# Performance work log

Measured on AMD Instinct MI355X. Metric: run time of the kernel, lower is better.

Reference implementation:

```python
import jax, jax.numpy as jnp
import numpy as np


def setup_inputs() -> dict:
    key = jax.random.key(0)
    ks = jax.random.split(key, 7)
    B, T, I, H, O = 64, 2048, 32, 256, 32
    s = 0.05
    return {
        "x": jax.random.normal(ks[0], (B, T, I), dtype=jnp.float32),
        "W_ih": jax.random.normal(ks[1], (4 * H, I), dtype=jnp.float32) * s,
        "W_hh": jax.random.normal(ks[2], (4 * H, H), dtype=jnp.float32) * s,
        "b_ih": jax.random.normal(ks[3], (4 * H,), dtype=jnp.float32) * s,
        "b_hh": jax.random.normal(ks[4], (4 * H,), dtype=jnp.float32) * s,
        "fc_w": jax.random.normal(ks[5], (O, H), dtype=jnp.float32) * s,
        "fc_b": jax.random.normal(ks[6], (O,), dtype=jnp.float32) * s,
    }


def _lstm(x, W_ih, W_hh, b_ih, b_hh):
    # x: [B,T,I]; PyTorch gate order: i, f, g, o stacked along 4H axis.
    B = x.shape[0]
    H = W_hh.shape[1]
    # Precompute input contributions for all timesteps in one GEMM: [B,T,4H]
    xg = jnp.einsum('bti,gi->btg', x, W_ih) + b_ih + b_hh

    def step(carry, xg_t):
        h, c = carry  # [B,H] each
        gates = xg_t + h @ W_hh.T  # [B,4H]
        i, f, g, o = jnp.split(gates, 4, axis=-1)
        i = jax.nn.sigmoid(i)
        f = jax.nn.sigmoid(f)
        g = jnp.tanh(g)
        o = jax.nn.sigmoid(o)
        c = f * c + i * g
        h = o * jnp.tanh(c)
        return (h, c), h

    h0 = jnp.zeros((B, H), dtype=x.dtype)
    (_, _), hs = jax.lax.scan(step, (h0, h0), jnp.swapaxes(xg, 0, 1))
    return jnp.swapaxes(hs, 0, 1)  # [B,T,H]


def reference(x, W_ih, W_hh, b_ih, b_hh, fc_w, fc_b):
    out = _lstm(x, W_ih, W_hh, b_ih, b_hh)          # [B,T,H]
    # Conv1d(H, O, kernel_size=1) over channel dim == pointwise linear.
    return jnp.einsum('bth,oh->bto', out, fc_w) + fc_b  # [B,T,O]
```

## Files before the change

### kernel.cpp

```cpp
#include <hip/hip_runtime.h>
#include <cstdint>


#define B_  64
#define T_  2048
#define I_  32
#define H_  256
#define G4  1024
#define O_  32

typedef int v16i __attribute__((ext_vector_type(16)));
typedef int v4i  __attribute__((ext_vector_type(4)));
typedef _Float16 h2_t __attribute__((ext_vector_type(2)));

#if __has_builtin(__builtin_amdgcn_sdot4)
__device__ __forceinline__ int dot4(int a, int b, int c) {
    return __builtin_amdgcn_sdot4(a, b, c, false);
}
#else
__device__ __forceinline__ int dot4(int a, int b, int c) {
    c += (int)(int8_t)(a)        * (int)(int8_t)(b);
    c += (int)(int8_t)(a >> 8)   * (int)(int8_t)(b >> 8);
    c += (int)(int8_t)(a >> 16)  * (int)(int8_t)(b >> 16);
    c += (int)(int8_t)(a >> 24)  * (int)(int8_t)(b >> 24);
    return c;
}
#endif

__device__ __forceinline__ float fdot2h(h2_t a, h2_t b, float c) {
#if __has_builtin(__builtin_amdgcn_fdot2)
    return __builtin_amdgcn_fdot2(a, b, c, false);
#else
    return c + (float)a[0] * (float)b[0] + (float)a[1] * (float)b[1];
#endif
}

#define QWHH_OFF 0
#define QWIH_OFF 262144
#define S1_OFF   327680
#define S2_OFF   331776
#define BIAS_OFF 335872
#define XQ_OFF   339968
#define XS_OFF   8728576
#define HBUF_OFF 9252864
#define HREC_STRIDE 320
#define HSLOTS 2049

__device__ __forceinline__ uint32_t pack_q(int q0, int q1, int q2, int q3) {
    return  ((uint32_t)(uint8_t)(int8_t)q0)
          | (((uint32_t)(uint8_t)(int8_t)q1) << 8)
          | (((uint32_t)(uint8_t)(int8_t)q2) << 16)
          | (((uint32_t)(uint8_t)(int8_t)q3) << 24);
}

__device__ __forceinline__ int clamp127(int v) {
    return v < -127 ? -127 : (v > 127 ? 127 : v);
}

__global__ __launch_bounds__(64) void prep_w(
    const float* __restrict__ Whh, const float* __restrict__ Wih,
    const float* __restrict__ bih, const float* __restrict__ bhh,
    uint32_t* __restrict__ qwhh, uint32_t* __restrict__ qwih,
    float* __restrict__ s1, float* __restrict__ s2, float* __restrict__ bias)
{
    const int r = blockIdx.x;
    const int l = threadIdx.x;

    const float4 wv = ((const float4*)(Whh + r * H_))[l];
    float m = fmaxf(fmaxf(fabsf(wv.x), fabsf(wv.y)), fmaxf(fabsf(wv.z), fabsf(wv.w)));
    #pragma unroll
    for (int s = 1; s < 64; s <<= 1) m = fmaxf(m, __shfl_xor(m, s, 64));
    const float S1 = fmaxf(m, 1e-20f) / 127.f;

    float xm = (l < I_) ? fabsf(Wih[r * I_ + l]) : 0.f;
    #pragma unroll
    for (int s = 1; s < 64; s <<= 1) xm = fmaxf(xm, __shfl_xor(xm, s, 64));
    const float S2 = fmaxf(xm, 1e-20f) / 127.f;

    {
        const float r1 = 1.f / S1;
        qwhh[l * G4 + r] = pack_q(
            clamp127((int)rintf(wv.x * r1)), clamp127((int)rintf(wv.y * r1)),
            clamp127((int)rintf(wv.z * r1)), clamp127((int)rintf(wv.w * r1)));
    }
    if (l < 8) {
        const float4 xw = ((const float4*)(Wih + r * I_))[l];
        const float r2 = 1.f / S2;
        qwih[l * G4 + r] = pack_q(
            clamp127((int)rintf(xw.x * r2)), clamp127((int)rintf(xw.y * r2)),
            clamp127((int)rintf(xw.z * r2)), clamp127((int)rintf(xw.w * r2)));
    } else if (l < 16) {
        const int j = l - 8;
        const float4 xw = ((const float4*)(Wih + r * I_))[j];
        const float r2 = 1.f / S2;
        float v0 = xw.x * r2, v1 = xw.y * r2, v2 = xw.z * r2, v3 = xw.w * r2;
        int a0 = clamp127((int)rintf(v0)), a1 = clamp127((int)rintf(v1));
        int a2 = clamp127((int)rintf(v2)), a3 = clamp127((int)rintf(v3));
        qwih[(8 + j) * G4 + r] = pack_q(
            clamp127((int)rintf((v0 - (float)a0) * 127.f)),
            clamp127((int)rintf((v1 - (float)a1) * 127.f)),
            clamp127((int)rintf((v2 - (float)a2) * 127.f)),
            clamp127((int)rintf((v3 - (float)a3) * 127.f)));
    }
    if (l == 0) { s1[r] = S1; s2[r] = S2; bias[r] = bih[r] + bhh[r]; }
}

__global__ __launch_bounds__(256) void prep_x(
    const float* __restrict__ x, uint32_t* __restrict__ xq, float* __restrict__ xs)
{
    __shared__ float xb[64 * 32];
    const int base = blockIdx.x * 64 * 32;
    for (int i = threadIdx.x; i < 2048; i += 256) xb[i] = x[base + i];
    __syncthreads();
    const int t = threadIdx.x;
    if (t < 64) {
        float m = 0.f;
        for (int k = 0; k < 32; k++) m = fmaxf(m, fabsf(xb[t * 32 + k]));
        const float S = fmaxf(m, 1e-20f) / 127.f;
        const int row = blockIdx.x * 64 + t;
        xs[row] = S;
        const float rS = 1.f / S;
        for (int j = 0; j < 8; j++) {
            int qa[4], qb[4];
            for (int e = 0; e < 4; e++) {
                float v = xb[t * 32 + j * 4 + e] * rS;
                int a = clamp127((int)rintf(v));
                int b = clamp127((int)rintf((v - (float)a) * 127.f));
                qa[e] = a; qb[e] = b;
            }
            xq[row * 16 + j]     = pack_q(qa[0], qa[1], qa[2], qa[3]);
            xq[row * 16 + 8 + j] = pack_q(qb[0], qb[1], qb[2], qb[3]);
        }
    }
}

__device__ __forceinline__ float x_contrib(const uint32_t* pxq, const float* pxs,
                                           const uint32_t* wA, const uint32_t* wB,
                                           float S2, float bias_r) {
    v16i xv; int sxi;
    asm volatile("s_load_dwordx16 %0, %2, 0x0\n\t"
                 "s_load_dword %1, %3, 0x0\n\t"
                 "s_waitcnt lgkmcnt(0)"
                 : "=&s"(xv), "=&s"(sxi)
                 : "s"(pxq), "s"(pxs)
                 : "memory");
    int aA = 0, aM = 0;
    #pragma unroll
    for (int j = 0; j < 8; j++) {
        aA = dot4((int)wA[j], xv[j],     aA);
        aM = dot4((int)wA[j], xv[8 + j], aM);
        aM = dot4((int)wB[j], xv[j],     aM);
    }
    return ((float)aA + (float)aM * (1.f / 127.f)) * (S2 * __int_as_float(sxi)) + bias_r;
}

__global__ __launch_bounds__(1024, 4) void lstm_main(
    const uint32_t* __restrict__ qwhh, const uint32_t* __restrict__ qwih,
    const float* __restrict__ s1v, const float* __restrict__ s2v,
    const float* __restrict__ biasv,
    const uint32_t* __restrict__ xq, const float* __restrict__ xs,
    const float* __restrict__ fcw, const float* __restrict__ fcb,
    char* __restrict__ hbuf, float* __restrict__ out)
{
    const int b   = blockIdx.x;
    const int tid = threadIdx.x;

    __shared__ float    gbuf[768];
    __shared__ uint32_t hf16[128];

    uint32_t w[64], wA[8], wB[8];
    #pragma unroll
    for (int d = 0; d < 64; d++) w[d] = qwhh[d * G4 + tid];
    #pragma unroll
    for (int j = 0; j < 8; j++) { wA[j] = qwih[j * G4 + tid]; wB[j] = qwih[(8 + j) * G4 + tid]; }
    const float S1 = s1v[tid], S2 = s2v[tid], bias_r = biasv[tid];

    const int o_ = tid >> 5, kc = tid & 31;
    h2_t fw[4];
    {
        const float* fr = fcw + o_ * H_ + kc * 8;
        #pragma unroll
        for (int j = 0; j < 4; j++) {
            h2_t p; p[0] = (_Float16)fr[2 * j]; p[1] = (_Float16)fr[2 * j + 1];
            fw[j] = p;
        }
    }
    const float fcb_v = fcb[o_];

    char* hb = hbuf + (size_t)b * (HSLOTS * HREC_STRIDE);
    if (tid < H_) hb[2048 * HREC_STRIDE + tid] = 0;
    if (tid >= 256 && tid < 260) ((float*)(hb + 2048 * HREC_STRIDE + 256))[tid - 256] = 0.f;

    const uint32_t* xqb  = xq + (size_t)(b * T_) * 16;
    const float*    xsb  = xs + (size_t)(b * T_);
    float*          outb = out + (size_t)(b * T_) * O_;

    float c_state = 0.f;
    float x_part  = x_contrib(xqb, xsb, wA, wB, S2, bias_r);

    __syncthreads();

    for (int t = 0; t < T_; t++) {
        const uint32_t slot = (t == 0) ? 2048u : ((uint32_t)(t * 1993) & 2047u);
        const char* hrec = hb + (size_t)slot * HREC_STRIDE;
        v16i h0, h1, h2, h3; v4i scv;
        asm volatile("s_load_dwordx16 %0, %5, 0x0\n\t"
                     "s_load_dwordx16 %1, %5, 0x40\n\t"
                     "s_load_dwordx16 %2, %5, 0x80\n\t"
                     "s_load_dwordx16 %3, %5, 0xc0\n\t"
                     "s_load_dwordx4  %4, %5, 0x100\n\t"
                     "s_waitcnt lgkmcnt(0)"
                     : "=&s"(h0), "=&s"(h1), "=&s"(h2), "=&s"(h3), "=&s"(scv)
                     : "s"(hrec)
                     : "memory");

        int a0 = 0, a1 = 0, a2 = 0, a3 = 0;
        #pragma unroll
        for (int d = 0; d < 16; d++) {
            a0 = dot4((int)w[d],      h0[d], a0);
            a1 = dot4((int)w[16 + d], h1[d], a1);
            a2 = dot4((int)w[32 + d], h2[d], a2);
            a3 = dot4((int)w[48 + d], h3[d], a3);
        }
        const float hsum = (float)a0 * __int_as_float(scv[0])
                         + (float)a1 * __int_as_float(scv[1])
                         + (float)a2 * __int_as_float(scv[2])
                         + (float)a3 * __int_as_float(scv[3]);
        const float gate = hsum * S1 + x_part;

        if (tid >= 256) gbuf[tid - 256] = gate;
        __syncthreads();

        const uint32_t wslot = (uint32_t)((t + 1) * 1993) & 2047u;
        char* hw = hb + (size_t)wslot * HREC_STRIDE;
        float hval = 0.f;
        if (tid < H_) {
            const float gi = gate;
            const float gf = gbuf[tid];
            const float gg = gbuf[256 + tid];
            const float go = gbuf[512 + tid];
            const float i_ = 1.f / (1.f + __expf(-gi));
            const float f_ = 1.f / (1.f + __expf(-gf));
            const float g_ = 2.f / (1.f + __expf(-2.f * gg)) - 1.f;
            const float oo = 1.f / (1.f + __expf(-go));
            c_state = f_ * c_state + i_ * g_;
            const float tc = 2.f / (1.f + __expf(-2.f * c_state)) - 1.f;
            hval = oo * tc;
            ((_Float16*)hf16)[tid] = (_Float16)hval;

            float m = fabsf(hval);
            #pragma unroll
            for (int s = 1; s < 64; s <<= 1) m = fmaxf(m, __shfl_xor(m, s, 64));
            m = fmaxf(m, 1e-12f);
            const float rq = 127.f / m;
            const int q = clamp127((int)rintf(hval * rq));
            hw[tid] = (char)(int8_t)q;
            if ((tid & 63) == 0)
                ((float*)(hw + 256))[tid >> 6] = m * (1.f / 127.f);
        }

        if (t < T_ - 1)
            x_part = x_contrib(xqb + (size_t)(t + 1) * 16, xsb + (t + 1),
                               wA, wB, S2, bias_r);

        __syncthreads();

        {
            const uint4 hv = *(const uint4*)(&hf16[4 * kc]);
            union { uint32_t u; h2_t h; } u0, u1, u2, u3;
            u0.u = hv.x; u1.u = hv.y; u2.u = hv.z; u3.u = hv.w;
            float acc = 0.f;
            acc = fdot2h(fw[0], u0.h, acc);
            acc = fdot2h(fw[1], u1.h, acc);
            acc = fdot2h(fw[2], u2.h, acc);
            acc = fdot2h(fw[3], u3.h, acc);
            #pragma unroll
            for (int s = 1; s < 32; s <<= 1) acc += __shfl_xor(acc, s, 64);
            if (kc == 0) outb[t * O_ + o_] = acc + fcb_v;
        }
    }
}

extern "C" void kernel_launch(void* const* d_in, const int* in_sizes, int n_in,
                              void* d_out, int out_size, void* d_ws, size_t ws_size,
                              hipStream_t stream) {
    const float* x    = (const float*)d_in[0];
    const float* Wih  = (const float*)d_in[1];
    const float* Whh  = (const float*)d_in[2];
    const float* bih  = (const float*)d_in[3];
    const float* bhh  = (const float*)d_in[4];
    const float* fcw  = (const float*)d_in[5];
    const float* fcb  = (const float*)d_in[6];
    float* out = (float*)d_out;

    char* ws = (char*)d_ws;
    uint32_t* qwhh = (uint32_t*)(ws + QWHH_OFF);
    uint32_t* qwih = (uint32_t*)(ws + QWIH_OFF);
    float*    s1   = (float*)(ws + S1_OFF);
    float*    s2   = (float*)(ws + S2_OFF);
    float*    bias = (float*)(ws + BIAS_OFF);
    uint32_t* xq   = (uint32_t*)(ws + XQ_OFF);
    float*    xs   = (float*)(ws + XS_OFF);
    char*     hbuf = ws + HBUF_OFF;

    prep_w<<<G4, 64, 0, stream>>>(Whh, Wih, bih, bhh, qwhh, qwih, s1, s2, bias);
    prep_x<<<(B_ * T_) / 64, 256, 0, stream>>>(x, xq, xs);
    lstm_main<<<B_, 1024, 0, stream>>>(qwhh, qwih, s1, s2, bias, xq, xs,
                                       fcw, fcb, hbuf, out);
}
```

Measured before the change: 3.533 ms.

## Halve LSTM block size, precompute input gates, split FC into separate kernel

The recurrent kernel now uses 512 threads per batch, each computing two gate rows (i/g or f/o paired across half-waves via shuffles). This removes the shared-memory gate exchange and one barrier per step, at the cost of doubling per-thread weight registers. When the workspace is large enough, the input projection is precomputed in fp16 by a separate GEMM kernel and streamed in per step. The output linear layer moves out of the recurrent loop into a batched fc_kernel over stored fp16 hidden states, which adds extra memory traffic and launches.

```diff
diff --git a/kernel.cpp b/kernel.cpp
--- a/kernel.cpp
+++ b/kernel.cpp
@@ -10,7 +10,7 @@
 #define O_  32
 
 typedef int v16i __attribute__((ext_vector_type(16)));
-typedef int v4i  __attribute__((ext_vector_type(4)));
+typedef int v8i  __attribute__((ext_vector_type(8)));
 typedef _Float16 h2_t __attribute__((ext_vector_type(2)));
 
 #if __has_builtin(__builtin_amdgcn_sdot4)
@@ -35,16 +35,20 @@
 #endif
 }
 
-#define QWHH_OFF 0
-#define QWIH_OFF 262144
-#define S1_OFF   327680
-#define S2_OFF   331776
-#define BIAS_OFF 335872
-#define XQ_OFF   339968
-#define XS_OFF   8728576
-#define HBUF_OFF 9252864
+#define QWHH_OFF 0u
+#define QWIH_OFF 262144u
+#define S1_OFF   327680u
+#define S2_OFF   331776u
+#define BIAS_OFF 335872u
+#define HBUF_OFF 339968u
 #define HREC_STRIDE 320
 #define HSLOTS 2049
+#define HSTORE_OFF (339968u + 41963520u)
+#define XQ_OFF  (HSTORE_OFF + 67108864u)
+#define XS_OFF  (XQ_OFF + 8388608u)
+#define XG_OFF  (HSTORE_OFF + 67108864u)
+#define FULL_NEED  ((size_t)XG_OFF + 268435456ull)
+#define FB_NEED    ((size_t)XS_OFF + 524288ull)
 
 __device__ __forceinline__ uint32_t pack_q(int q0, int q1, int q2, int q3) {
     return  ((uint32_t)(uint8_t)(int8_t)q0)
@@ -52,10 +56,10 @@
           | (((uint32_t)(uint8_t)(int8_t)q2) << 16)
           | (((uint32_t)(uint8_t)(int8_t)q3) << 24);
 }
-
 __device__ __forceinline__ int clamp127(int v) {
     return v < -127 ? -127 : (v > 127 ? 127 : v);
 }
+
 
 __global__ __launch_bounds__(64) void prep_w(
     const float* __restrict__ Whh, const float* __restrict__ Wih,
@@ -65,6 +69,10 @@
 {
     const int r = blockIdx.x;
     const int l = threadIdx.x;
+    const int j = r & 255, g = r >> 8;
+    const int col = 64 * (j >> 5) + ((g & 1) ? 32 : 0) + (j & 31);
+    const int dbase = (g >= 2) ? 64 : 0;
+    const int xbase = (g >= 2) ? 16 : 0;
 
     const float4 wv = ((const float4*)(Whh + r * H_))[l];
     float m = fmaxf(fmaxf(fabsf(wv.x), fabsf(wv.y)), fmaxf(fabsf(wv.z), fabsf(wv.w)));
@@ -79,30 +87,77 @@
 
     {
         const float r1 = 1.f / S1;
-        qwhh[l * G4 + r] = pack_q(
+        qwhh[(dbase + l) * 512 + col] = pack_q(
             clamp127((int)rintf(wv.x * r1)), clamp127((int)rintf(wv.y * r1)),
             clamp127((int)rintf(wv.z * r1)), clamp127((int)rintf(wv.w * r1)));
     }
     if (l < 8) {
         const float4 xw = ((const float4*)(Wih + r * I_))[l];
         const float r2 = 1.f / S2;
-        qwih[l * G4 + r] = pack_q(
+        qwih[(xbase + l) * 512 + col] = pack_q(
             clamp127((int)rintf(xw.x * r2)), clamp127((int)rintf(xw.y * r2)),
             clamp127((int)rintf(xw.z * r2)), clamp127((int)rintf(xw.w * r2)));
     } else if (l < 16) {
-        const int j = l - 8;
-        const float4 xw = ((const float4*)(Wih + r * I_))[j];
+        const int jj = l - 8;
+        const float4 xw = ((const float4*)(Wih + r * I_))[jj];
         const float r2 = 1.f / S2;
         float v0 = xw.x * r2, v1 = xw.y * r2, v2 = xw.z * r2, v3 = xw.w * r2;
         int a0 = clamp127((int)rintf(v0)), a1 = clamp127((int)rintf(v1));
         int a2 = clamp127((int)rintf(v2)), a3 = clamp127((int)rintf(v3));
-        qwih[(8 + j) * G4 + r] = pack_q(
+        qwih[(xbase + 8 + jj) * 512 + col] = pack_q(
             clamp127((int)rintf((v0 - (float)a0) * 127.f)),
             clamp127((int)rintf((v1 - (float)a1) * 127.f)),
             clamp127((int)rintf((v2 - (float)a2) * 127.f)),
             clamp127((int)rintf((v3 - (float)a3) * 127.f)));
     }
     if (l == 0) { s1[r] = S1; s2[r] = S2; bias[r] = bih[r] + bhh[r]; }
+}
+
+__global__ __launch_bounds__(512, 4) void gemm_xg(
+    const float* __restrict__ x, const float* __restrict__ Wih,
+    const float* __restrict__ biasv, uint32_t* __restrict__ xg)
+{
+    const int b  = blockIdx.x >> 3;
+    const int t0 = (blockIdx.x & 7) * 256;
+    const int tid = threadIdx.x;
+    const int w_ = tid >> 6, l = tid & 63;
+    const int j = 32 * w_ + (l & 31);
+    const bool up = (l >= 32);
+    const int rowA = up ? 256 + j : j;
+    const int rowB = up ? 768 + j : 512 + j;
+
+    float wa[32], wb[32];
+    #pragma unroll
+    for (int k4 = 0; k4 < 8; k4++) {
+        const float4 va = ((const float4*)(Wih + rowA * I_))[k4];
+        const float4 vb = ((const float4*)(Wih + rowB * I_))[k4];
+        wa[4*k4] = va.x; wa[4*k4+1] = va.y; wa[4*k4+2] = va.z; wa[4*k4+3] = va.w;
+        wb[4*k4] = vb.x; wb[4*k4+1] = vb.y; wb[4*k4+2] = vb.z; wb[4*k4+3] = vb.w;
+    }
+    const float biasA = biasv[rowA], biasB = biasv[rowB];
+
+    for (int tt = 0; tt < 256; tt++) {
+        const float* xrow = x + ((size_t)b * T_ + t0 + tt) * I_;
+        v16i x0, x1;
+        asm volatile("s_load_dwordx16 %0, %2, 0x0\n\t"
+                     "s_load_dwordx16 %1, %2, 0x40\n\t"
+                     "s_waitcnt lgkmcnt(0)"
+                     : "=&s"(x0), "=&s"(x1) : "s"(xrow) : "memory");
+        float a = biasA, bsum = biasB;
+        #pragma unroll
+        for (int k = 0; k < 16; k++) {
+            a    = fmaf(wa[k], __int_as_float(x0[k]), a);
+            bsum = fmaf(wb[k], __int_as_float(x0[k]), bsum);
+        }
+        #pragma unroll
+        for (int k = 0; k < 16; k++) {
+            a    = fmaf(wa[16+k], __int_as_float(x1[k]), a);
+            bsum = fmaf(wb[16+k], __int_as_float(x1[k]), bsum);
+        }
+        union { h2_t h; uint32_t u; } cv;
+        cv.h[0] = (_Float16)a; cv.h[1] = (_Float16)bsum;
+        xg[((size_t)b * T_ + t0 + tt) * 512 + tid] = cv.u;
+    }
 }
 
 __global__ __launch_bounds__(256) void prep_x(
@@ -120,165 +175,219 @@
         const int row = blockIdx.x * 64 + t;
         xs[row] = S;
         const float rS = 1.f / S;
-        for (int j = 0; j < 8; j++) {
+        for (int jj = 0; jj < 8; jj++) {
             int qa[4], qb[4];
             for (int e = 0; e < 4; e++) {
-                float v = xb[t * 32 + j * 4 + e] * rS;
+                float v = xb[t * 32 + jj * 4 + e] * rS;
                 int a = clamp127((int)rintf(v));
                 int b = clamp127((int)rintf((v - (float)a) * 127.f));
                 qa[e] = a; qb[e] = b;
             }
-            xq[row * 16 + j]     = pack_q(qa[0], qa[1], qa[2], qa[3]);
-            xq[row * 16 + 8 + j] = pack_q(qb[0], qb[1], qb[2], qb[3]);
-        }
-    }
-}
-
-__device__ __forceinline__ float x_contrib(const uint32_t* pxq, const float* pxs,
-                                           const uint32_t* wA, const uint32_t* wB,
-                                           float S2, float bias_r) {
-    v16i xv; int sxi;
-    asm volatile("s_load_dwordx16 %0, %2, 0x0\n\t"
-                 "s_load_dword %1, %3, 0x0\n\t"
-                 "s_waitcnt lgkmcnt(0)"
-                 : "=&s"(xv), "=&s"(sxi)
-                 : "s"(pxq), "s"(pxs)
-                 : "memory");
-    int aA = 0, aM = 0;
-    #pragma unroll
-    for (int j = 0; j < 8; j++) {
-        aA = dot4((int)wA[j], xv[j],     aA);
-        aM = dot4((int)wA[j], xv[8 + j], aM);
-        aM = dot4((int)wB[j], xv[j],     aM);
-    }
-    return ((float)aA + (float)aM * (1.f / 127.f)) * (S2 * __int_as_float(sxi)) + bias_r;
-}
-
-__global__ __launch_bounds__(1024, 4) void lstm_main(
+            xq[row * 16 + jj]     = pack_q(qa[0], qa[1], qa[2], qa[3]);
+            xq[row * 16 + 8 + jj] = pack_q(qb[0], qb[1], qb[2], qb[3]);
+        }
+    }
+}
+
+#define GRP(GACC, WOFF, HV, HOFF, SC) { int acc_ = 0; \
+    acc_ = dot4((int)w[(WOFF)+0], HV[(HOFF)+0], acc_); \
+    acc_ = dot4((int)w[(WOFF)+1], HV[(HOFF)+1], acc_); \
+    acc_ = dot4((int)w[(WOFF)+2], HV[(HOFF)+2], acc_); \
+    acc_ = dot4((int)w[(WOFF)+3], HV[(HOFF)+3], acc_); \
+    acc_ = dot4((int)w[(WOFF)+4], HV[(HOFF)+4], acc_); \
+    acc_ = dot4((int)w[(WOFF)+5], HV[(HOFF)+5], acc_); \
+    acc_ = dot4((int)w[(WOFF)+6], HV[(HOFF)+6], acc_); \
+    acc_ = dot4((int)w[(WOFF)+7], HV[(HOFF)+7], acc_); \
+    GACC = fmaf((float)acc_, (SC), GACC); }
+
+template<bool USE_XG>
+__global__ __launch_bounds__(512, 2) void lstm_main(
     const uint32_t* __restrict__ qwhh, const uint32_t* __restrict__ qwih,
     const float* __restrict__ s1v, const float* __restrict__ s2v,
     const float* __restrict__ biasv,
+    const uint32_t* __restrict__ xg,
     const uint32_t* __restrict__ xq, const float* __restrict__ xs,
-    const float* __restrict__ fcw, const float* __restrict__ fcb,
-    char* __restrict__ hbuf, float* __restrict__ out)
+    char* __restrict__ hbuf, _Float16* __restrict__ hstore)
 {
     const int b   = blockIdx.x;
     const int tid = threadIdx.x;
-
-    __shared__ float    gbuf[768];
-    __shared__ uint32_t hf16[128];
-
-    uint32_t w[64], wA[8], wB[8];
-    #pragma unroll
-    for (int d = 0; d < 64; d++) w[d] = qwhh[d * G4 + tid];
-    #pragma unroll
-    for (int j = 0; j < 8; j++) { wA[j] = qwih[j * G4 + tid]; wB[j] = qwih[(8 + j) * G4 + tid]; }
-    const float S1 = s1v[tid], S2 = s2v[tid], bias_r = biasv[tid];
-
-    const int o_ = tid >> 5, kc = tid & 31;
-    h2_t fw[4];
-    {
-        const float* fr = fcw + o_ * H_ + kc * 8;
+    const int w_  = tid >> 6, l = tid & 63;
+    const int j   = 32 * w_ + (l & 31);
+    const bool up = (l >= 32);
+    const int rowA = up ? 256 + j : j;
+    const int rowB = up ? 768 + j : 512 + j;
+
+    uint32_t w[128];
+    #pragma unroll
+    for (int d = 0; d < 128; d++) w[d] = qwhh[d * 512 + tid];
+    const float S1A = s1v[rowA], S1B = s1v[rowB];
+
+    uint32_t wxa[16], wxb[16];
+    float S2A = 0.f, S2B = 0.f, biasA = 0.f, biasB = 0.f;
+    if (!USE_XG) {
         #pragma unroll
-        for (int j = 0; j < 4; j++) {
-            h2_t p; p[0] = (_Float16)fr[2 * j]; p[1] = (_Float16)fr[2 * j + 1];
-            fw[j] = p;
-        }
-    }
-    const float fcb_v = fcb[o_];
-
-    char* hb = hbuf + (size_t)b * (HSLOTS * HREC_STRIDE);
-    if (tid < H_) hb[2048 * HREC_STRIDE + tid] = 0;
-    if (tid >= 256 && tid < 260) ((float*)(hb + 2048 * HREC_STRIDE + 256))[tid - 256] = 0.f;
-
-    const uint32_t* xqb  = xq + (size_t)(b * T_) * 16;
-    const float*    xsb  = xs + (size_t)(b * T_);
-    float*          outb = out + (size_t)(b * T_) * O_;
+        for (int k = 0; k < 16; k++) {
+            wxa[k] = qwih[k * 512 + tid];
+            wxb[k] = qwih[(16 + k) * 512 + tid];
+        }
+        S2A = s2v[rowA]; S2B = s2v[rowB];
+        biasA = biasv[rowA]; biasB = biasv[rowB];
+    }
+
+    char* hb = hbuf + (size_t)b * ((size_t)HSLOTS * HREC_STRIDE);
+    if (tid < 72) ((uint32_t*)(hb + 2048 * HREC_STRIDE))[tid] = 0u;
+
+    const uint32_t* xgb = USE_XG ? (xg + (size_t)b * T_ * 512 + tid) : nullptr;
+    const uint32_t* xqb = xq + (size_t)b * T_ * 16;
+    const float*    xsb = xs + (size_t)b * T_;
+    _Float16*       hsb = hstore + (size_t)b * T_ * H_;
 
     float c_state = 0.f;
-    float x_part  = x_contrib(xqb, xsb, wA, wB, S2, bias_r);
-
+    uint32_t xg_cur = 0;
+    if (USE_XG) xg_cur = xgb[0];
     __syncthreads();
 
     for (int t = 0; t < T_; t++) {
         const uint32_t slot = (t == 0) ? 2048u : ((uint32_t)(t * 1993) & 2047u);
         const char* hrec = hb + (size_t)slot * HREC_STRIDE;
-        v16i h0, h1, h2, h3; v4i scv;
+        v16i h0, h1, h2, h3; v8i scv;
         asm volatile("s_load_dwordx16 %0, %5, 0x0\n\t"
                      "s_load_dwordx16 %1, %5, 0x40\n\t"
                      "s_load_dwordx16 %2, %5, 0x80\n\t"
                      "s_load_dwordx16 %3, %5, 0xc0\n\t"
-                     "s_load_dwordx4  %4, %5, 0x100\n\t"
+                     "s_load_dwordx8  %4, %5, 0x100\n\t"
                      "s_waitcnt lgkmcnt(0)"
                      : "=&s"(h0), "=&s"(h1), "=&s"(h2), "=&s"(h3), "=&s"(scv)
                      : "s"(hrec)
                      : "memory");
 
-        int a0 = 0, a1 = 0, a2 = 0, a3 = 0;
-        #pragma unroll
-        for (int d = 0; d < 16; d++) {
-            a0 = dot4((int)w[d],      h0[d], a0);
-            a1 = dot4((int)w[16 + d], h1[d], a1);
-            a2 = dot4((int)w[32 + d], h2[d], a2);
-            a3 = dot4((int)w[48 + d], h3[d], a3);
-        }
-        const float hsum = (float)a0 * __int_as_float(scv[0])
-                         + (float)a1 * __int_as_float(scv[1])
-                         + (float)a2 * __int_as_float(scv[2])
-                         + (float)a3 * __int_as_float(scv[3]);
-        const float gate = hsum * S1 + x_part;
-
-        if (tid >= 256) gbuf[tid - 256] = gate;
-        __syncthreads();
+        uint32_t xg_nxt = 0;
+        if (USE_XG && t + 1 < T_) xg_nxt = xgb[(size_t)(t + 1) * 512];
+
+        float xA, xB;
+        if (USE_XG) {
+            union { uint32_t u; h2_t h; } cv; cv.u = xg_cur;
+            xA = (float)cv.h[0]; xB = (float)cv.h[1];
+        } else {
+            v16i xv; int sxi;
+            const uint32_t* pxq = xqb + (size_t)t * 16;
+            const float*    pxs = xsb + t;
+            asm volatile("s_load_dwordx16 %0, %2, 0x0\n\t"
+                         "s_load_dword %1, %3, 0x0\n\t"
+                         "s_waitcnt lgkmcnt(0)"
+                         : "=&s"(xv), "=&s"(sxi) : "s"(pxq), "s"(pxs) : "memory");
+            int aA = 0, aM = 0, bA = 0, bM = 0;
+            #pragma unroll
+            for (int k = 0; k < 8; k++) {
+                aA = dot4((int)wxa[k],     xv[k],     aA);
+                aM = dot4((int)wxa[8 + k], xv[k],     aM);
+                aM = dot4((int)wxa[k],     xv[8 + k], aM);
+                bA = dot4((int)wxb[k],     xv[k],     bA);
+                bM = dot4((int)wxb[8 + k], xv[k],     bM);
+                bM = dot4((int)wxb[k],     xv[8 + k], bM);
+            }
+            const float Sx = __int_as_float(sxi);
+            xA = ((float)aA + (float)aM * (1.f/127.f)) * (S2A * Sx) + biasA;
+            xB = ((float)bA + (float)bM * (1.f/127.f)) * (S2B * Sx) + biasB;
+        }
+
+        float gaccA = 0.f;
+        GRP(gaccA,  0, h0, 0, __int_as_float(scv[0]));
+        GRP(gaccA,  8, h0, 8, __int_as_float(scv[1]));
+        GRP(gaccA, 16, h1, 0, __int_as_float(scv[2]));
+        GRP(gaccA, 24, h1, 8, __int_as_float(scv[3]));
+        GRP(gaccA, 32, h2, 0, __int_as_float(scv[4]));
+        GRP(gaccA, 40, h2, 8, __int_as_float(scv[5]));
+        GRP(gaccA, 48, h3, 0, __int_as_float(scv[6]));
+        GRP(gaccA, 56, h3, 8, __int_as_float(scv[7]));
+        float gaccB = 0.f;
+        GRP(gaccB,  64, h0, 0, __int_as_float(scv[0]));
+        GRP(gaccB,  72, h0, 8, __int_as_float(scv[1]));
+        GRP(gaccB,  80, h1, 0, __int_as_float(scv[2]));
+        GRP(gaccB,  88, h1, 8, __int_as_float(scv[3]));
+        GRP(gaccB,  96, h2, 0, __int_as_float(scv[4]));
+        GRP(gaccB, 104, h2, 8, __int_as_float(scv[5]));
+        GRP(gaccB, 112, h3, 0, __int_as_float(scv[6]));
+        GRP(gaccB, 120, h3, 8, __int_as_float(scv[7]));
+
+        const float gateA = gaccA * S1A + xA;
+        const float gateB = gaccB * S1B + xB;
+
+        const float gF = __shfl_xor(gateA, 32, 64);
+        const float gO = __shfl_xor(gateB, 32, 64);
 
         const uint32_t wslot = (uint32_t)((t + 1) * 1993) & 2047u;
         char* hw = hb + (size_t)wslot * HREC_STRIDE;
-        float hval = 0.f;
-        if (tid < H_) {
-            const float gi = gate;
-            const float gf = gbuf[tid];
-            const float gg = gbuf[256 + tid];
-            const float go = gbuf[512 + tid];
-            const float i_ = 1.f / (1.f + __expf(-gi));
-            const float f_ = 1.f / (1.f + __expf(-gf));
-            const float g_ = 2.f / (1.f + __expf(-2.f * gg)) - 1.f;
-            const float oo = 1.f / (1.f + __expf(-go));
+
+        if (l < 32) {
+            const float i_ = 1.f / (1.f + __expf(-gateA));
+            const float g_ = 2.f / (1.f + __expf(-2.f * gateB)) - 1.f;
+            const float f_ = 1.f / (1.f + __expf(-gF));
+            const float o_ = 1.f / (1.f + __expf(-gO));
             c_state = f_ * c_state + i_ * g_;
             const float tc = 2.f / (1.f + __expf(-2.f * c_state)) - 1.f;
-            hval = oo * tc;
-            ((_Float16*)hf16)[tid] = (_Float16)hval;
+            const float hval = o_ * tc;
+            hsb[(size_t)t * H_ + j] = (_Float16)hval;
 
             float m = fabsf(hval);
             #pragma unroll
-            for (int s = 1; s < 64; s <<= 1) m = fmaxf(m, __shfl_xor(m, s, 64));
+            for (int s = 1; s < 32; s <<= 1) m = fmaxf(m, __shfl_xor(m, s, 64));
             m = fmaxf(m, 1e-12f);
-            const float rq = 127.f / m;
-            const int q = clamp127((int)rintf(hval * rq));
-            hw[tid] = (char)(int8_t)q;
-            if ((tid & 63) == 0)
-                ((float*)(hw + 256))[tid >> 6] = m * (1.f / 127.f);
-        }
-
-        if (t < T_ - 1)
-            x_part = x_contrib(xqb + (size_t)(t + 1) * 16, xsb + (t + 1),
-                               wA, wB, S2, bias_r);
-
+            const int q = clamp127((int)rintf(hval * (127.f / m)));
+            hw[j] = (char)(int8_t)q;
+            if ((l & 31) == 0) ((float*)(hw + 256))[w_] = m * (1.f / 127.f);
+        }
+        xg_cur = xg_nxt;
         __syncthreads();
-
-        {
-            const uint4 hv = *(const uint4*)(&hf16[4 * kc]);
-            union { uint32_t u; h2_t h; } u0, u1, u2, u3;
-            u0.u = hv.x; u1.u = hv.y; u2.u = hv.z; u3.u = hv.w;
-            float acc = 0.f;
-            acc = fdot2h(fw[0], u0.h, acc);
-            acc = fdot2h(fw[1], u1.h, acc);
-            acc = fdot2h(fw[2], u2.h, acc);
-            acc = fdot2h(fw[3], u3.h, acc);
-            #pragma unroll
-            for (int s = 1; s < 32; s <<= 1) acc += __shfl_xor(acc, s, 64);
-            if (kc == 0) outb[t * O_ + o_] = acc + fcb_v;
-        }
-    }
+    }
+}
+
+__global__ __launch_bounds__(256) void fc_kernel(
+    const uint32_t* __restrict__ hstore_u,
+    const float* __restrict__ fcw, const float* __restrict__ fcb,
+    float* __restrict__ out)
+{
+    __shared__ uint32_t hlds[64 * 128];
+    __shared__ uint32_t wlds[32 * 32 * 4];
+    const int rb = blockIdx.x * 64;
+    const uint4* src = (const uint4*)(hstore_u + (size_t)rb * 128);
+    for (int i = threadIdx.x; i < 2048; i += 256) ((uint4*)hlds)[i] = src[i];
+    for (int i = threadIdx.x; i < 4096; i += 256) {
+        const int o = i >> 7, kp = i & 127;
+        union { h2_t h; uint32_t u; } cv;
+        cv.h[0] = (_Float16)fcw[o * 256 + 2 * kp];
+        cv.h[1] = (_Float16)fcw[o * 256 + 2 * kp + 1];
+        wlds[((kp >> 2) * 32 + o) * 4 + (kp & 3)] = cv.u;
+    }
+    __syncthreads();
+
+    const int o = threadIdx.x & 31, rg = threadIdx.x >> 5;
+    const float bv = fcb[o];
+    float acc[8];
+    #pragma unroll
+    for (int rr = 0; rr < 8; rr++) acc[rr] = bv;
+
+    for (int ch = 0; ch < 32; ch++) {
+        const uint4 wv = *(const uint4*)(wlds + (ch * 32 + o) * 4);
+        union { uint32_t u; h2_t h; } w0, w1, w2, w3;
+        w0.u = wv.x; w1.u = wv.y; w2.u = wv.z; w3.u = wv.w;
+        #pragma unroll
+        for (int rr = 0; rr < 8; rr++) {
+            const int row = rg * 8 + rr;
+            const uint4 hv = *(const uint4*)(hlds + row * 128 + ch * 4);
+            union { uint32_t u; h2_t h; } x0, x1, x2, x3;
+            x0.u = hv.x; x1.u = hv.y; x2.u = hv.z; x3.u = hv.w;
+            float a = acc[rr];
+            a = fdot2h(w0.h, x0.h, a);
+            a = fdot2h(w1.h, x1.h, a);
+            a = fdot2h(w2.h, x2.h, a);
+            a = fdot2h(w3.h, x3.h, a);
+            acc[rr] = a;
+        }
+    }
+    #pragma unroll
+    for (int rr = 0; rr < 8; rr++)
+        out[(size_t)(rb + rg * 8 + rr) * O_ + o] = acc[rr];
 }
 
 extern "C" void kernel_launch(void* const* d_in, const int* in_sizes, int n_in,
@@ -299,12 +408,23 @@
     float*    s1   = (float*)(ws + S1_OFF);
     float*    s2   = (float*)(ws + S2_OFF);
     float*    bias = (float*)(ws + BIAS_OFF);
-    uint32_t* xq   = (uint32_t*)(ws + XQ_OFF);
-    float*    xs   = (float*)(ws + XS_OFF);
     char*     hbuf = ws + HBUF_OFF;
+    _Float16* hstore = (_Float16*)(ws + HSTORE_OFF);
+    uint32_t* xqp  = (uint32_t*)(ws + XQ_OFF);
+    float*    xsp  = (float*)(ws + XS_OFF);
+    uint32_t* xgp  = (uint32_t*)(ws + XG_OFF);
+
+    const bool use_xg = (ws_size >= FULL_NEED);
 
     prep_w<<<G4, 64, 0, stream>>>(Whh, Wih, bih, bhh, qwhh, qwih, s1, s2, bias);
-    prep_x<<<(B_ * T_) / 64, 256, 0, stream>>>(x, xq, xs);
-    lstm_main<<<B_, 1024, 0, stream>>>(qwhh, qwih, s1, s2, bias, xq, xs,
-                                       fcw, fcb, hbuf, out);
-}
+    if (use_xg) {
+        gemm_xg<<<512, 512, 0, stream>>>(x, Wih, bias, xgp);
+        lstm_main<true><<<B_, 512, 0, stream>>>(qwhh, qwih, s1, s2, bias,
+                                                xgp, nullptr, nullptr, hbuf, hstore);
+    } else {
+        prep_x<<<(B_ * T_) / 64, 256, 0, stream>>>(x, xqp, xsp);
+        lstm_main<false><<<B_, 512, 0, stream>>>(qwhh, qwih, s1, s2, bias,
+                                                 nullptr, xqp, xsp, hbuf, hstore);
+    }
+    fc_kernel<<<(B_ * T_) / 64, 256, 0, stream>>>((const uint32_t*)hstore, fcw, fcb, out);
+}
```

Result: slower. 4.507 ms (+27.6%).
